# Kernel optimization log

Hardware: AMD Instinct MI355X
Metric: run time of the kernel (lower is better)

The kernel has to match this reference:

```python
import jax, jax.numpy as jnp
import numpy as np

B, S, E, H = 2, 2048, 1024, 16
D = E // H  # head_dim = 64


def setup_inputs() -> dict:
    key = jax.random.key(0)
    ks = jax.random.split(key, 12)
    sc = 1.0 / np.sqrt(E)
    inp = {
        "query": jax.random.normal(ks[0], (B, S, E), jnp.float32),
        "key": jax.random.normal(ks[1], (B, S, E), jnp.float32),
        "value": jax.random.normal(ks[2], (B, S, E), jnp.float32),
        # causal mask: 1 where attending is allowed, 0 where blocked
        "mask": jnp.tril(jnp.ones((S, S), jnp.int32))[None, None, :, :],
        "Wq": jax.random.normal(ks[3], (E, E), jnp.float32) * sc,
        "bq": jax.random.normal(ks[4], (E,), jnp.float32) * sc,
        "Wk": jax.random.normal(ks[5], (E, E), jnp.float32) * sc,
        "bk": jax.random.normal(ks[6], (E,), jnp.float32) * sc,
        "Wv": jax.random.normal(ks[7], (E, E), jnp.float32) * sc,
        "bv": jax.random.normal(ks[8], (E,), jnp.float32) * sc,
        "Wo": jax.random.normal(ks[9], (E, E), jnp.float32) * sc,
        "bo": jax.random.normal(ks[10], (E,), jnp.float32) * sc,
    }
    return inp


def reference(query, key, value, mask, Wq, bq, Wk, bk, Wv, bv, Wo, bo):
    scale = jnp.asarray(np.sqrt(D), query.dtype)
    # Linear projections (torch Linear: x @ W.T + b)
    Q = query @ Wq.T + bq
    K = key @ Wk.T + bk
    V = value @ Wv.T + bv
    # [B, S, E] -> [B, H, S, D]
    Q = Q.reshape(B, -1, H, D).transpose(0, 2, 1, 3)
    K = K.reshape(B, -1, H, D).transpose(0, 2, 1, 3)
    V = V.reshape(B, -1, H, D).transpose(0, 2, 1, 3)
    # full [B, H, Sq, Sk] score matrix, as in the source
    scores = jnp.einsum("bhqd,bhkd->bhqk", Q, K) / scale
    scores = jnp.where(mask == 0, jnp.asarray(-1e10, scores.dtype), scores)
    weights = jax.nn.softmax(scores, axis=-1)
    weighted = jnp.einsum("bhqk,bhkd->bhqd", weights, V)
    concat = weighted.transpose(0, 2, 1, 3).reshape(B, -1, E)
    return concat @ Wo.T + bo
```

## Files before the change

### kernel.cpp

```cpp
#include <hip/hip_runtime.h>
#include <math.h>

#define BB 2
#define SS 2048
#define EE 1024
#define HH 16
#define DD 64

typedef unsigned short u16;
typedef __attribute__((ext_vector_type(8))) short short8;
typedef __attribute__((ext_vector_type(4))) float f32x4;

__device__ __forceinline__ u16 f2bf(float x) {
    union { float f; unsigned u; } v; v.f = x;
    return (u16)((v.u + 0x7fffu + ((v.u >> 16) & 1u)) >> 16);
}

__device__ __forceinline__ float exp2_fast(float x) {
    float r;
    asm("v_exp_f32 %0, %1" : "=v"(r) : "v"(x));
    return r;
}

#define GLL16(gp, lp) \
    __builtin_amdgcn_global_load_lds( \
        (const __attribute__((address_space(1))) void*)(gp), \
        (__attribute__((address_space(3))) void*)(lp), 16, 0, 0)

#define BARRIER do { asm volatile("" ::: "memory"); \
                     __builtin_amdgcn_s_barrier();  \
                     asm volatile("" ::: "memory"); } while (0)
#define VMW4 asm volatile("s_waitcnt vmcnt(4)" ::: "memory")
#define VMW0 asm volatile("s_waitcnt vmcnt(0)" ::: "memory")
#define LG0  asm volatile("s_waitcnt lgkmcnt(0)" ::: "memory")
#define SCHED0 __builtin_amdgcn_sched_barrier(0)

#define QSCALE 0.18033688f

__global__ __launch_bounds__(256)
void cvt_bf16(const float* __restrict__ s0, const float* __restrict__ s1,
              const float* __restrict__ s2, const float* __restrict__ s3,
              u16* __restrict__ d0, u16* __restrict__ d1,
              u16* __restrict__ d2, u16* __restrict__ d3)
{
    const int z = blockIdx.y;
    const float* s; u16* d;
    switch (z) {
        case 0: s = s0; d = d0; break;
        case 1: s = s1; d = d1; break;
        case 2: s = s2; d = d2; break;
        default: s = s3; d = d3; break;
    }
    const int i = (blockIdx.x * 256 + threadIdx.x) * 8;
    float4 a = *(const float4*)(s + i);
    float4 b = *(const float4*)(s + i + 4);
    short8 r;
    r[0] = (short)f2bf(a.x); r[1] = (short)f2bf(a.y);
    r[2] = (short)f2bf(a.z); r[3] = (short)f2bf(a.w);
    r[4] = (short)f2bf(b.x); r[5] = (short)f2bf(b.y);
    r[6] = (short)f2bf(b.z); r[7] = (short)f2bf(b.w);
    *(short8*)(d + i) = r;
}

__global__ __launch_bounds__(256, 3)
void gemm_qkv(const float* __restrict__ Xq, const float* __restrict__ Xk,
              const float* __restrict__ Xv,
              const u16* __restrict__ Wqb, const u16* __restrict__ Wkb,
              const u16* __restrict__ Wvb,
              const float* __restrict__ bq, const float* __restrict__ bk,
              const float* __restrict__ bv,
              u16* __restrict__ Qh, u16* __restrict__ Kh, u16* __restrict__ Vth)
{
    __shared__ __align__(16) u16 LS[2][2][128][32];
#define LA (LS[0])
#define LB (LS[1])

    const int bid = blockIdx.x;
    const int swz = (bid & 7) * 96 + (bid >> 3);
    const int z   = swz >> 8;
    const int rem = swz & 255;
    const int m0  = (rem >> 3) * 128;
    const int n0  = (rem & 7) * 128;

    const float* X = (z == 0) ? Xq : (z == 1) ? Xk : Xv;
    const u16* Wt = (z == 0) ? Wqb : (z == 1) ? Wkb : Wvb;
    const float* bias = (z == 0) ? bq : (z == 1) ? bk : bv;
    u16* out = (z == 0) ? Qh : (z == 1) ? Kh : Vth;

    const int t = threadIdx.x;
    const int w = t >> 6, l = t & 63;
    const int ln = l & 15, hi = l >> 4;
    const int wr = w >> 1, wc = w & 1;

    const int ar = t >> 1, ah = t & 1;
    const float* Xrow = X + (size_t)(m0 + ar) * 1024 + ah * 16;
    const int fa   = (ar >> 1) & 3;
    const int gpa0 = (2 * ah)     ^ fa;
    const int gpa1 = (2 * ah + 1) ^ fa;

    const int brow = t >> 2, gp4 = t & 3;
    const int gl4  = gp4 ^ (brow & 3);
    const u16* Wp0 = Wt + (size_t)(n0 + brow) * 1024 + gl4 * 8;
    const u16* Wp1 = Wt + (size_t)(n0 + 64 + brow) * 1024 + gl4 * 8;

    f32x4 acc[4][4];
    #pragma unroll
    for (int i = 0; i < 4; i++)
        #pragma unroll
        for (int j = 0; j < 4; j++)
            acc[i][j] = (f32x4){0.f, 0.f, 0.f, 0.f};

    float4 e0, e1, e2, e3;
    float4 o0, o1, o2, o3;

#define ISSUE_B(buf, k0_) {                                                  \
        GLL16(Wp0 + (k0_), &LB[buf][brow][gp4 * 8]);                         \
        GLL16(Wp1 + (k0_), &LB[buf][brow + 64][gp4 * 8]);                    \
    }
#define LOAD_A(S0, S1, S2, S3, k0_) {                                        \
        S0 = *(const float4*)(Xrow + (k0_));                                 \
        S1 = *(const float4*)(Xrow + (k0_) + 4);                             \
        S2 = *(const float4*)(Xrow + (k0_) + 8);                             \
        S3 = *(const float4*)(Xrow + (k0_) + 12);                            \
    }
#define CVT_A(buf, S0, S1, S2, S3) {                                         \
        uint4 u0, u1;                                                        \
        u0.x = f2bf(S0.x) | ((unsigned)f2bf(S0.y) << 16);                    \
        u0.y = f2bf(S0.z) | ((unsigned)f2bf(S0.w) << 16);                    \
        u0.z = f2bf(S1.x) | ((unsigned)f2bf(S1.y) << 16);                    \
        u0.w = f2bf(S1.z) | ((unsigned)f2bf(S1.w) << 16);                    \
        u1.x = f2bf(S2.x) | ((unsigned)f2bf(S2.y) << 16);                    \
        u1.y = f2bf(S2.z) | ((unsigned)f2bf(S2.w) << 16);                    \
        u1.z = f2bf(S3.x) | ((unsigned)f2bf(S3.y) << 16);                    \
        u1.w = f2bf(S3.z) | ((unsigned)f2bf(S3.w) << 16);                    \
        *(uint4*)&LA[buf][ar][gpa0 * 8] = u0;                                \
        *(uint4*)&LA[buf][ar][gpa1 * 8] = u1;                                \
    }
#define COMPUTE(la_, lb_, SW) {                                              \
        _Pragma("unroll")                                                    \
        for (int mi = 0; mi < 4; mi++)                                       \
            af[mi] = *(const short8*)&LA[la_][wr*64 + mi*16 + ln]            \
                         [(hi ^ ((ln >> 1) & 3)) * 8];                       \
        _Pragma("unroll")                                                    \
        for (int nj = 0; nj < 4; nj++)                                       \
            bf[nj] = *(const short8*)&LB[lb_][wc*64 + nj*16 + ln]            \
                         [(hi ^ (ln & 3)) * 8];                              \
        _Pragma("unroll")                                                    \
        for (int mi = 0; mi < 4; mi++)                                       \
            _Pragma("unroll")                                                \
            for (int nj = 0; nj < 4; nj++)                                   \
                acc[mi][nj] = (SW)                                           \
                    ? __builtin_amdgcn_mfma_f32_16x16x32_bf16(               \
                          bf[nj], af[mi], acc[mi][nj], 0, 0, 0)              \
                    : __builtin_amdgcn_mfma_f32_16x16x32_bf16(               \
                          af[mi], bf[nj], acc[mi][nj], 0, 0, 0);             \
    }
#define PIPELINE(SW)                                                         \
    LOAD_A(e0, e1, e2, e3, 0);                                               \
    CVT_A(0, e0, e1, e2, e3);                                                \
    ISSUE_B(0, 0); SCHED0;                                                   \
    LOAD_A(o0, o1, o2, o3, 32); SCHED0;                                      \
    VMW4; LG0; BARRIER;                                                      \
    for (int it = 0; it < 15; ++it) {                                        \
        const int k0 = it * 64;                                              \
        ISSUE_B(1, k0 + 32); SCHED0;                                         \
        LOAD_A(e0, e1, e2, e3, k0 + 64); SCHED0;                             \
        COMPUTE(0, 0, SW);                                                   \
        CVT_A(1, o0, o1, o2, o3);                                            \
        VMW4; LG0; BARRIER;                                                  \
        ISSUE_B(0, k0 + 64); SCHED0;                                         \
        LOAD_A(o0, o1, o2, o3, k0 + 96); SCHED0;                             \
        COMPUTE(1, 1, SW);                                                   \
        CVT_A(0, e0, e1, e2, e3);                                            \
        VMW4; LG0; BARRIER;                                                  \
    }                                                                        \
    ISSUE_B(1, 992); SCHED0;                                                 \
    COMPUTE(0, 0, SW);                                                       \
    CVT_A(1, o0, o1, o2, o3);                                                \
    VMW0; LG0; BARRIER;                                                      \
    COMPUTE(1, 1, SW);

    short8 af[4], bf[4];

    if (z == 2) { PIPELINE(0) } else { PIPELINE(1) }
#undef ISSUE_B
#undef LOAD_A
#undef CVT_A
#undef COMPUTE
#undef PIPELINE

    u16* T = &LS[0][0][0][0];
    const int b = m0 >> 11;

    if (z == 2) {
        #pragma unroll
        for (int mi = 0; mi < 4; mi++) {
            #pragma unroll
            for (int nj = 0; nj < 4; nj++) {
                const int nc = wc * 64 + nj * 16 + ln;
                const float bv2 = bias[n0 + nc];
                const int sr0 = wr * 64 + mi * 16 + hi * 4;
                uint2 pk;
                pk.x = f2bf(acc[mi][nj][0] + bv2)
                     | ((unsigned)f2bf(acc[mi][nj][1] + bv2) << 16);
                pk.y = f2bf(acc[mi][nj][2] + bv2)
                     | ((unsigned)f2bf(acc[mi][nj][3] + bv2) << 16);
                const int gp = (sr0 >> 2) ^ (nc & 31);
                *(uint2*)&T[nc * 128 + gp * 4] = pk;
            }
        }
        __syncthreads();
        const int s0 = m0 & 2047;
        const int sidx = t & 15;
        const int ncr0 = t >> 4;
        #pragma unroll
        for (int i = 0; i < 8; i++) {
            const int nc = ncr0 + i * 16;
            const int a  = sidx * 2;
            const int pa = a ^ (nc & 31);
            const int pb = (a + 1) ^ (nc & 31);
            uint2 lo  = *(const uint2*)&T[nc * 128 + pa * 4];
            uint2 hi2 = *(const uint2*)&T[nc * 128 + pb * 4];
            uint4 vd = make_uint4(lo.x, lo.y, hi2.x, hi2.y);
            const int h = (n0 >> 6) + (nc >> 6);
            const int d = nc & 63;
            *(uint4*)&out[(((size_t)(b * HH + h) * 64 + d) << 11) + s0 + sidx * 8] = vd;
        }
    } else {
        #pragma unroll
        for (int mi = 0; mi < 4; mi++) {
            const int s = (m0 & 2047) + wr * 64 + mi * 16 + ln;
            #pragma unroll
            for (int nj = 0; nj < 4; nj++) {
                const int ncb = wc * 64 + nj * 16 + hi * 4;
                float4 b4 = *(const float4*)&bias[n0 + ncb];
                float v0 = acc[mi][nj][0] + b4.x;
                float v1 = acc[mi][nj][1] + b4.y;
                float v2 = acc[mi][nj][2] + b4.z;
                float v3 = acc[mi][nj][3] + b4.w;
                if (z == 0) {
                    v0 *= QSCALE; v1 *= QSCALE; v2 *= QSCALE; v3 *= QSCALE;
                }
                const int h  = (n0 + ncb) >> 6;
                const int d0 = ncb & 63;
                uint2 pk;
                pk.x = f2bf(v0) | ((unsigned)f2bf(v1) << 16);
                pk.y = f2bf(v2) | ((unsigned)f2bf(v3) << 16);
                *(uint2*)&out[((((size_t)(b * HH + h)) << 11) + s) * 64 + d0] = pk;
            }
        }
    }
#undef LA
#undef LB
}

__global__ __launch_bounds__(256)
void gemm_out(const u16* __restrict__ Xb, const u16* __restrict__ Wb,
              const float* __restrict__ bias, float* __restrict__ outp)
{
    __shared__ __align__(16) u16 As[2][64][32];
    __shared__ __align__(16) u16 Bs[2][128][32];

    const int bid = blockIdx.x;
    const int swz = (bid & 7) * 64 + (bid >> 3);
    const int m0  = (swz >> 3) * 64;
    const int n0  = (swz & 7) * 128;

    const int t = threadIdx.x;
    const int w = t >> 6, l = t & 63;
    const int ln = l & 15, hi = l >> 4;
    const int wr = w >> 1, wc = w & 1;

    const int row0 = t >> 2, gp4 = t & 3;
    const int gl4  = gp4 ^ (row0 & 3);

    f32x4 acc[2][4];
    #pragma unroll
    for (int i = 0; i < 2; i++)
        #pragma unroll
        for (int j = 0; j < 4; j++)
            acc[i][j] = (f32x4){0.f, 0.f, 0.f, 0.f};

#define OSTAGE(buf, k0_) { \
    GLL16(Xb + (size_t)(m0 + row0) * 1024 + (k0_) + gl4 * 8,        \
          &As[buf][row0][gp4 * 8]);                                  \
    GLL16(Wb + (size_t)(n0 + row0) * 1024 + (k0_) + gl4 * 8,        \
          &Bs[buf][row0][gp4 * 8]);                                  \
    GLL16(Wb + (size_t)(n0 + 64 + row0) * 1024 + (k0_) + gl4 * 8,   \
          &Bs[buf][row0 + 64][gp4 * 8]); }

    OSTAGE(0, 0);
    __syncthreads();
    int cur = 0;
    for (int k0 = 0; k0 < 1024; k0 += 32) {
        if (k0 + 32 < 1024) OSTAGE(cur ^ 1, k0 + 32);
        short8 af[2], bfr[4];
        #pragma unroll
        for (int mi = 0; mi < 2; mi++)
            af[mi] = *(const short8*)&As[cur][wr*32 + mi*16 + ln][(hi ^ (ln & 3))*8];
        #pragma unroll
        for (int nj = 0; nj < 4; nj++)
            bfr[nj] = *(const short8*)&Bs[cur][wc*64 + nj*16 + ln][(hi ^ (ln & 3))*8];
        #pragma unroll
        for (int mi = 0; mi < 2; mi++)
            #pragma unroll
            for (int nj = 0; nj < 4; nj++)
                acc[mi][nj] = __builtin_amdgcn_mfma_f32_16x16x32_bf16(
                    bfr[nj], af[mi], acc[mi][nj], 0, 0, 0);
        __syncthreads();
        cur ^= 1;
    }
#undef OSTAGE

    #pragma unroll
    for (int mi = 0; mi < 2; mi++) {
        const int m = m0 + wr * 32 + mi * 16 + ln;
        #pragma unroll
        for (int nj = 0; nj < 4; nj++) {
            const int nb0 = n0 + wc * 64 + nj * 16 + hi * 4;
            float4 b4 = *(const float4*)&bias[nb0];
            float4 st;
            st.x = acc[mi][nj][0] + b4.x;
            st.y = acc[mi][nj][1] + b4.y;
            st.z = acc[mi][nj][2] + b4.z;
            st.w = acc[mi][nj][3] + b4.w;
            *(float4*)&outp[(size_t)m * 1024 + nb0] = st;
        }
    }
}

__global__ __launch_bounds__(256)
void attn_mfma(const u16* __restrict__ Qh, const u16* __restrict__ Kh,
               const u16* __restrict__ Vt, u16* __restrict__ Cc)
{
    __shared__ __align__(16) u16 Ks[2][2][4][64][8];
    __shared__ __align__(16) u16 Vs[2][2][4][64][8];
    __shared__ __align__(16) u16 Ps[4][16][64];
    const int bh = blockIdx.x;
    const int y  = 31 - blockIdx.y;
    const int q0 = y * 64;
    const int t = threadIdx.x, w = t >> 6, l = t & 63;
    const int ln = l & 15, hi = l >> 4;
    const size_t base = (size_t)bh * SS * DD;
    const int qg = q0 + w * 16 + ln;

    short8 qf0, qf1;
    {
        const u16* qp = Qh + base + (size_t)qg * 64 + hi * 8;
        qf0 = *(const short8*)qp;
        qf1 = *(const short8*)(qp + 32);
    }
    f32x4 o[4];
    #pragma unroll
    for (int dj = 0; dj < 4; dj++) o[dj] = (f32x4){0.f, 0.f, 0.f, 0.f};
    float mrun = -INFINITY, lrun = 0.f;

#define STAGE(buf, key0_)                                                        \
    {                                                                            \
        _Pragma("unroll")                                                        \
        for (int i_ = 0; i_ < 4; i_++) {                                         \
            const int id_ = w + i_ * 4;                                          \
            if (id_ < 8) {                                                       \
                const int dc_ = id_ >> 2, kg_ = id_ & 3;                         \
                const u16* gp_ = Kh + base + (size_t)((key0_) + l) * 64          \
                                 + dc_ * 32 + kg_ * 8;                           \
                GLL16(gp_, &Ks[buf][dc_][kg_][0][0]);                            \
            } else {                                                             \
                const int kc_ = (id_ >> 2) & 1, kg_ = id_ & 3;                   \
                const u16* gp_ = Vt + base + (size_t)l * SS + (key0_)            \
                                 + kc_ * 32 + kg_ * 8;                           \
                GLL16(gp_, &Vs[buf][kc_][kg_][0][0]);                            \
            }                                                                    \
        }                                                                        \
    }

    STAGE(0, 0);
    __syncthreads();
    int cur = 0;
    const int nkt = y + 1;
    for (int kt = 0; kt < nkt; kt++) {
        const int key0 = kt * 64;
        if (kt + 1 < nkt) STAGE(cur ^ 1, key0 + 64);

        f32x4 st[4];
        __builtin_amdgcn_s_setprio(1);
        #pragma unroll
        for (int kt4 = 0; kt4 < 4; kt4++) {
            short8 ka = *(const short8*)&Ks[cur][0][hi][kt4 * 16 + ln][0];
            short8 kb = *(const short8*)&Ks[cur][1][hi][kt4 * 16 + ln][0];
            f32x4 zz = (f32x4){0.f, 0.f, 0.f, 0.f};
            zz = __builtin_amdgcn_mfma_f32_16x16x32_bf16(ka, qf0, zz, 0, 0, 0);
            zz = __builtin_amdgcn_mfma_f32_16x16x32_bf16(kb, qf1, zz, 0, 0, 0);
            st[kt4] = zz;
        }
        __builtin_amdgcn_s_setprio(0);
        if (kt == y) {
            #pragma unroll
            for (int kt4 = 0; kt4 < 4; kt4++)
                #pragma unroll
                for (int r = 0; r < 4; r++)
                    if (key0 + kt4 * 16 + hi * 4 + r > qg)
                        st[kt4][r] = -INFINITY;
        }

        float tmax = -INFINITY;
        #pragma unroll
        for (int kt4 = 0; kt4 < 4; kt4++)
            #pragma unroll
            for (int r = 0; r < 4; r++)
                tmax = fmaxf(tmax, st[kt4][r]);
        tmax = fmaxf(tmax, __shfl_xor(tmax, 16));
        tmax = fmaxf(tmax, __shfl_xor(tmax, 32));
        if (__ballot(tmax > mrun + 8.f)) {
            const float mnew = fmaxf(mrun, tmax);
            const float alpha = exp2_fast(mrun - mnew);
            lrun *= alpha;
            mrun = mnew;
            #pragma unroll
            for (int r = 0; r < 4; r++) {
                const float ar = __shfl(alpha, hi * 4 + r);
                #pragma unroll
                for (int dj = 0; dj < 4; dj++) o[dj][r] *= ar;
            }
        }
        float p[4][4];
        float lsum = 0.f;
        #pragma unroll
        for (int kt4 = 0; kt4 < 4; kt4++)
            #pragma unroll
            for (int r = 0; r < 4; r++) {
                p[kt4][r] = exp2_fast(st[kt4][r] - mrun);
                lsum += p[kt4][r];
            }
        lsum += __shfl_xor(lsum, 16);
        lsum += __shfl_xor(lsum, 32);
        lrun += lsum;

        char* prow = ((char*)Ps) + (w * 16 + ln) * 128 + (hi & 1) * 8;
        #pragma unroll
        for (int kt4 = 0; kt4 < 4; kt4++) {
            unsigned dw0, dw1;
            asm("v_cvt_pk_bf16_f32 %0, %1, %2" : "=v"(dw0)
                : "v"(p[kt4][0]), "v"(p[kt4][1]));
            asm("v_cvt_pk_bf16_f32 %0, %1, %2" : "=v"(dw1)
                : "v"(p[kt4][2]), "v"(p[kt4][3]));
            const int g = (2 * kt4 + (hi >> 1)) ^ (ln & 7);
            *(uint2*)(prow + g * 16) = make_uint2(dw0, dw1);
        }

        __builtin_amdgcn_s_setprio(1);
        #pragma unroll
        for (int kc = 0; kc < 2; kc++) {
            const int gr = (kc * 4 + hi) ^ (ln & 7);
            short8 pa = *(const short8*)(((char*)Ps) + (w * 16 + ln) * 128 + gr * 16);
            #pragma unroll
            for (int dj = 0; dj < 4; dj++) {
                short8 vb = *(const short8*)&Vs[cur][kc][hi][dj * 16 + ln][0];
                o[dj] = __builtin_amdgcn_mfma_f32_16x16x32_bf16(pa, vb, o[dj], 0, 0, 0);
            }
        }
        __builtin_amdgcn_s_setprio(0);
        __syncthreads();
        cur ^= 1;
    }
#undef STAGE

    const float inv = 1.f / lrun;
    #pragma unroll
    for (int r = 0; r < 4; r++) {
        const float ir = __shfl(inv, hi * 4 + r);
        const int s = q0 + w * 16 + hi * 4 + r;
        const size_t ob = ((size_t)(bh >> 4) * SS + s) * EE + (bh & 15) * 64;
        #pragma unroll
        for (int dj = 0; dj < 4; dj++)
            Cc[ob + dj * 16 + ln] = f2bf(o[dj][r] * ir);
    }
}

extern "C" void kernel_launch(void* const* d_in, const int* in_sizes, int n_in,
                              void* d_out, int out_size, void* d_ws, size_t ws_size,
                              hipStream_t stream)
{
    (void)in_sizes; (void)n_in; (void)out_size; (void)ws_size;
    const float* query = (const float*)d_in[0];
    const float* key   = (const float*)d_in[1];
    const float* value = (const float*)d_in[2];
    const float* Wq = (const float*)d_in[4];
    const float* bq = (const float*)d_in[5];
    const float* Wk = (const float*)d_in[6];
    const float* bk = (const float*)d_in[7];
    const float* Wv = (const float*)d_in[8];
    const float* bv = (const float*)d_in[9];
    const float* Wo = (const float*)d_in[10];
    const float* bo = (const float*)d_in[11];
    float* out = (float*)d_out;

    char* ws = (char*)d_ws;
    u16* Wqb = (u16*)(ws + 25165824);
    u16* Wkb = (u16*)(ws + 27262976);
    u16* Wvb = (u16*)(ws + 29360128);
    u16* Wob = (u16*)(ws + 31457280);
    u16* Qh  = (u16*)(ws + 33554432);
    u16* Kh  = (u16*)(ws + 41943040);
    u16* Vth = (u16*)(ws + 50331648);
    u16* Cc  = (u16*)(ws + 58720256);

    cvt_bf16<<<dim3(512, 4), 256, 0, stream>>>(
        Wq, Wk, Wv, Wo, Wqb, Wkb, Wvb, Wob);

    gemm_qkv<<<768, 256, 0, stream>>>(
        query, key, value, Wqb, Wkb, Wvb, bq, bk, bv, Qh, Kh, Vth);
    attn_mfma<<<dim3(32, 32), 256, 0, stream>>>(Qh, Kh, Vth, Cc);
    gemm_out<<<512, 256, 0, stream>>>(Cc, Wob, bo, out);
}
```

Before: 118.8 us.

## Process two 64-row query tiles per attention block to reuse K/V tiles

Each attention workgroup now handles 128 query rows: every wave keeps two 16-row Q fragments, two online-softmax states and two output accumulators. Each staged K/V tile is then reused for twice as many MFMAs, halving global/LDS staging per unit of work. Block-to-tile mapping is reordered to interleave long and short causal rows for load balance. The grid halves to 512 blocks and per-thread register use roughly doubles, which may lower occupancy and leave fewer blocks than CUs for latency hiding.

```diff
diff --git a/kernel.cpp b/kernel.cpp
--- a/kernel.cpp
+++ b/kernel.cpp
@@ -335,25 +335,34 @@
 {
     __shared__ __align__(16) u16 Ks[2][2][4][64][8];
     __shared__ __align__(16) u16 Vs[2][2][4][64][8];
-    __shared__ __align__(16) u16 Ps[4][16][64];
+    __shared__ __align__(16) u16 Ps[4][2][16][64];
     const int bh = blockIdx.x;
-    const int y  = 31 - blockIdx.y;
-    const int q0 = y * 64;
+    const int by = blockIdx.y;
+    const int y  = (by < 8) ? (15 - 2 * by) : (2 * (by - 8));
+    const int q0 = y * 128;
     const int t = threadIdx.x, w = t >> 6, l = t & 63;
     const int ln = l & 15, hi = l >> 4;
     const size_t base = (size_t)bh * SS * DD;
-    const int qg = q0 + w * 16 + ln;
-
-    short8 qf0, qf1;
+    const int qga = q0 + w * 16 + ln;
+    const int qgb = qga + 64;
+
+    short8 qf0, qf1, qf2, qf3;
     {
-        const u16* qp = Qh + base + (size_t)qg * 64 + hi * 8;
+        const u16* qp = Qh + base + (size_t)qga * 64 + hi * 8;
         qf0 = *(const short8*)qp;
         qf1 = *(const short8*)(qp + 32);
-    }
-    f32x4 o[4];
+        const u16* qp2 = qp + (size_t)64 * 64;
+        qf2 = *(const short8*)qp2;
+        qf3 = *(const short8*)(qp2 + 32);
+    }
+    f32x4 oa[4], ob[4];
     #pragma unroll
-    for (int dj = 0; dj < 4; dj++) o[dj] = (f32x4){0.f, 0.f, 0.f, 0.f};
-    float mrun = -INFINITY, lrun = 0.f;
+    for (int dj = 0; dj < 4; dj++) {
+        oa[dj] = (f32x4){0.f, 0.f, 0.f, 0.f};
+        ob[dj] = (f32x4){0.f, 0.f, 0.f, 0.f};
+    }
+    float m0r = -INFINITY, l0r = 0.f;
+    float m1r = -INFINITY, l1r = 0.f;
 
 #define STAGE(buf, key0_)                                                        \
     {                                                                            \
@@ -377,86 +386,109 @@
     STAGE(0, 0);
     __syncthreads();
     int cur = 0;
-    const int nkt = y + 1;
+    const int nkt = 2 * y + 2;
     for (int kt = 0; kt < nkt; kt++) {
         const int key0 = kt * 64;
         if (kt + 1 < nkt) STAGE(cur ^ 1, key0 + 64);
 
-        f32x4 st[4];
+        f32x4 st0[4], st1[4];
         __builtin_amdgcn_s_setprio(1);
         #pragma unroll
         for (int kt4 = 0; kt4 < 4; kt4++) {
             short8 ka = *(const short8*)&Ks[cur][0][hi][kt4 * 16 + ln][0];
             short8 kb = *(const short8*)&Ks[cur][1][hi][kt4 * 16 + ln][0];
-            f32x4 zz = (f32x4){0.f, 0.f, 0.f, 0.f};
-            zz = __builtin_amdgcn_mfma_f32_16x16x32_bf16(ka, qf0, zz, 0, 0, 0);
-            zz = __builtin_amdgcn_mfma_f32_16x16x32_bf16(kb, qf1, zz, 0, 0, 0);
-            st[kt4] = zz;
+            f32x4 z0 = (f32x4){0.f, 0.f, 0.f, 0.f};
+            z0 = __builtin_amdgcn_mfma_f32_16x16x32_bf16(ka, qf0, z0, 0, 0, 0);
+            z0 = __builtin_amdgcn_mfma_f32_16x16x32_bf16(kb, qf1, z0, 0, 0, 0);
+            st0[kt4] = z0;
+            f32x4 z1 = (f32x4){0.f, 0.f, 0.f, 0.f};
+            z1 = __builtin_amdgcn_mfma_f32_16x16x32_bf16(ka, qf2, z1, 0, 0, 0);
+            z1 = __builtin_amdgcn_mfma_f32_16x16x32_bf16(kb, qf3, z1, 0, 0, 0);
+            st1[kt4] = z1;
         }
         __builtin_amdgcn_s_setprio(0);
-        if (kt == y) {
+
+        if (kt >= nkt - 2) {
             #pragma unroll
             for (int kt4 = 0; kt4 < 4; kt4++)
                 #pragma unroll
-                for (int r = 0; r < 4; r++)
-                    if (key0 + kt4 * 16 + hi * 4 + r > qg)
-                        st[kt4][r] = -INFINITY;
-        }
-
-        float tmax = -INFINITY;
+                for (int r = 0; r < 4; r++) {
+                    const int key = key0 + kt4 * 16 + hi * 4 + r;
+                    if (key > qga) st0[kt4][r] = -INFINITY;
+                    if (key > qgb) st1[kt4][r] = -INFINITY;
+                }
+        }
+
+        float t0 = -INFINITY, t1 = -INFINITY;
         #pragma unroll
         for (int kt4 = 0; kt4 < 4; kt4++)
             #pragma unroll
-            for (int r = 0; r < 4; r++)
-                tmax = fmaxf(tmax, st[kt4][r]);
-        tmax = fmaxf(tmax, __shfl_xor(tmax, 16));
-        tmax = fmaxf(tmax, __shfl_xor(tmax, 32));
-        if (__ballot(tmax > mrun + 8.f)) {
-            const float mnew = fmaxf(mrun, tmax);
-            const float alpha = exp2_fast(mrun - mnew);
-            lrun *= alpha;
-            mrun = mnew;
-            #pragma unroll
             for (int r = 0; r < 4; r++) {
-                const float ar = __shfl(alpha, hi * 4 + r);
+                t0 = fmaxf(t0, st0[kt4][r]);
+                t1 = fmaxf(t1, st1[kt4][r]);
+            }
+        t0 = fmaxf(t0, __shfl_xor(t0, 16));
+        t0 = fmaxf(t0, __shfl_xor(t0, 32));
+        t1 = fmaxf(t1, __shfl_xor(t1, 16));
+        t1 = fmaxf(t1, __shfl_xor(t1, 32));
+        if (__ballot((t0 > m0r + 8.f) || (t1 > m1r + 8.f))) {
+            const float mn0 = fmaxf(m0r, t0);
+            const float mn1 = fmaxf(m1r, t1);
+            const float a0 = exp2_fast(m0r - mn0);
+            const float a1 = exp2_fast(m1r - mn1);
+            l0r *= a0; l1r *= a1;
+            m0r = mn0; m1r = mn1;
+            #pragma unroll
+            for (int r = 0; r < 4; r++) {
+                const float ar0 = __shfl(a0, hi * 4 + r);
+                const float ar1 = __shfl(a1, hi * 4 + r);
                 #pragma unroll
-                for (int dj = 0; dj < 4; dj++) o[dj][r] *= ar;
+                for (int dj = 0; dj < 4; dj++) {
+                    oa[dj][r] *= ar0;
+                    ob[dj][r] *= ar1;
+                }
             }
         }
-        float p[4][4];
-        float lsum = 0.f;
-        #pragma unroll
-        for (int kt4 = 0; kt4 < 4; kt4++)
+        float lsum0 = 0.f, lsum1 = 0.f;
+        char* prow0 = ((char*)&Ps[w][0][0][0]) + ln * 128 + (hi & 1) * 8;
+        char* prow1 = ((char*)&Ps[w][1][0][0]) + ln * 128 + (hi & 1) * 8;
+        #pragma unroll
+        for (int kt4 = 0; kt4 < 4; kt4++) {
+            float p0[4], p1[4];
             #pragma unroll
             for (int r = 0; r < 4; r++) {
-                p[kt4][r] = exp2_fast(st[kt4][r] - mrun);
-                lsum += p[kt4][r];
+                p0[r] = exp2_fast(st0[kt4][r] - m0r);
+                p1[r] = exp2_fast(st1[kt4][r] - m1r);
+                lsum0 += p0[r];
+                lsum1 += p1[r];
             }
-        lsum += __shfl_xor(lsum, 16);
-        lsum += __shfl_xor(lsum, 32);
-        lrun += lsum;
-
-        char* prow = ((char*)Ps) + (w * 16 + ln) * 128 + (hi & 1) * 8;
-        #pragma unroll
-        for (int kt4 = 0; kt4 < 4; kt4++) {
-            unsigned dw0, dw1;
-            asm("v_cvt_pk_bf16_f32 %0, %1, %2" : "=v"(dw0)
-                : "v"(p[kt4][0]), "v"(p[kt4][1]));
-            asm("v_cvt_pk_bf16_f32 %0, %1, %2" : "=v"(dw1)
-                : "v"(p[kt4][2]), "v"(p[kt4][3]));
+            unsigned dw0, dw1, dw2, dw3;
+            asm("v_cvt_pk_bf16_f32 %0, %1, %2" : "=v"(dw0) : "v"(p0[0]), "v"(p0[1]));
+            asm("v_cvt_pk_bf16_f32 %0, %1, %2" : "=v"(dw1) : "v"(p0[2]), "v"(p0[3]));
+            asm("v_cvt_pk_bf16_f32 %0, %1, %2" : "=v"(dw2) : "v"(p1[0]), "v"(p1[1]));
+            asm("v_cvt_pk_bf16_f32 %0, %1, %2" : "=v"(dw3) : "v"(p1[2]), "v"(p1[3]));
             const int g = (2 * kt4 + (hi >> 1)) ^ (ln & 7);
-            *(uint2*)(prow + g * 16) = make_uint2(dw0, dw1);
-        }
+            *(uint2*)(prow0 + g * 16) = make_uint2(dw0, dw1);
+            *(uint2*)(prow1 + g * 16) = make_uint2(dw2, dw3);
+        }
+        lsum0 += __shfl_xor(lsum0, 16);
+        lsum0 += __shfl_xor(lsum0, 32);
+        lsum1 += __shfl_xor(lsum1, 16);
+        lsum1 += __shfl_xor(lsum1, 32);
+        l0r += lsum0;
+        l1r += lsum1;
 
         __builtin_amdgcn_s_setprio(1);
         #pragma unroll
         for (int kc = 0; kc < 2; kc++) {
             const int gr = (kc * 4 + hi) ^ (ln & 7);
-            short8 pa = *(const short8*)(((char*)Ps) + (w * 16 + ln) * 128 + gr * 16);
+            short8 pa0 = *(const short8*)(((char*)&Ps[w][0][0][0]) + ln * 128 + gr * 16);
+            short8 pa1 = *(const short8*)(((char*)&Ps[w][1][0][0]) + ln * 128 + gr * 16);
             #pragma unroll
             for (int dj = 0; dj < 4; dj++) {
                 short8 vb = *(const short8*)&Vs[cur][kc][hi][dj * 16 + ln][0];
-                o[dj] = __builtin_amdgcn_mfma_f32_16x16x32_bf16(pa, vb, o[dj], 0, 0, 0);
+                oa[dj] = __builtin_amdgcn_mfma_f32_16x16x32_bf16(pa0, vb, oa[dj], 0, 0, 0);
+                ob[dj] = __builtin_amdgcn_mfma_f32_16x16x32_bf16(pa1, vb, ob[dj], 0, 0, 0);
             }
         }
         __builtin_amdgcn_s_setprio(0);
@@ -465,15 +497,20 @@
     }
 #undef STAGE
 
-    const float inv = 1.f / lrun;
+    const float inv0 = 1.f / l0r;
+    const float inv1 = 1.f / l1r;
     #pragma unroll
     for (int r = 0; r < 4; r++) {
-        const float ir = __shfl(inv, hi * 4 + r);
+        const float ir0 = __shfl(inv0, hi * 4 + r);
+        const float ir1 = __shfl(inv1, hi * 4 + r);
         const int s = q0 + w * 16 + hi * 4 + r;
-        const size_t ob = ((size_t)(bh >> 4) * SS + s) * EE + (bh & 15) * 64;
-        #pragma unroll
-        for (int dj = 0; dj < 4; dj++)
-            Cc[ob + dj * 16 + ln] = f2bf(o[dj][r] * ir);
+        const size_t ob0 = ((size_t)(bh >> 4) * SS + s) * EE + (bh & 15) * 64;
+        const size_t ob1 = ((size_t)(bh >> 4) * SS + s + 64) * EE + (bh & 15) * 64;
+        #pragma unroll
+        for (int dj = 0; dj < 4; dj++) {
+            Cc[ob0 + dj * 16 + ln] = f2bf(oa[dj][r] * ir0);
+            Cc[ob1 + dj * 16 + ln] = f2bf(ob[dj][r] * ir1);
+        }
     }
 }
 
@@ -510,6 +547,6 @@
 
     gemm_qkv<<<768, 256, 0, stream>>>(
         query, key, value, Wqb, Wkb, Wvb, bq, bk, bv, Qh, Kh, Vth);
-    attn_mfma<<<dim3(32, 32), 256, 0, stream>>>(Qh, Kh, Vth, Cc);
+    attn_mfma<<<dim3(32, 16), 256, 0, stream>>>(Qh, Kh, Vth, Cc);
     gemm_out<<<512, 256, 0, stream>>>(Cc, Wob, bo, out);
 }
```

After: 123.0 us. +3.5%, slower.

## Deepen QKV GEMM pipeline to triple-buffered B tiles and three A register stages

Applied to the files above, without the earlier changes.

Restructures the QKV projection GEMM main loop from a double-buffered scheme to triple-buffered LDS for the weight tile, with three sets of fp32 A-operand registers. Global loads are issued further ahead, and vmcnt waits are relaxed so more memory traffic stays in flight behind the MFMA work. In exchange it uses more registers and LDS per block, which may reduce occupancy under the 3-blocks-per-CU launch bound. The loop is fully restaged with a 6-step rotation and a hand-written epilogue.

```diff
diff --git a/kernel.cpp b/kernel.cpp
--- a/kernel.cpp
+++ b/kernel.cpp
@@ -30,9 +30,10 @@
 #define BARRIER do { asm volatile("" ::: "memory"); \
                      __builtin_amdgcn_s_barrier();  \
                      asm volatile("" ::: "memory"); } while (0)
-#define VMW4 asm volatile("s_waitcnt vmcnt(4)" ::: "memory")
-#define VMW0 asm volatile("s_waitcnt vmcnt(0)" ::: "memory")
-#define LG0  asm volatile("s_waitcnt lgkmcnt(0)" ::: "memory")
+#define VMW10 asm volatile("s_waitcnt vmcnt(10)" ::: "memory")
+#define VMW6  asm volatile("s_waitcnt vmcnt(6)" ::: "memory")
+#define VMW0  asm volatile("s_waitcnt vmcnt(0)" ::: "memory")
+#define LG0   asm volatile("s_waitcnt lgkmcnt(0)" ::: "memory")
 #define SCHED0 __builtin_amdgcn_sched_barrier(0)
 
 #define QSCALE 0.18033688f
@@ -71,9 +72,10 @@
               const float* __restrict__ bv,
               u16* __restrict__ Qh, u16* __restrict__ Kh, u16* __restrict__ Vth)
 {
-    __shared__ __align__(16) u16 LS[2][2][128][32];
-#define LA (LS[0])
-#define LB (LS[1])
+    __shared__ __align__(16) u16 LS[20480];
+    typedef u16 tile_t[128][32];
+    tile_t* LA = (tile_t*)&LS[0];
+    tile_t* LB = (tile_t*)&LS[8192];
 
     const int bid = blockIdx.x;
     const int swz = (bid & 7) * 96 + (bid >> 3);
@@ -112,6 +114,7 @@
 
     float4 e0, e1, e2, e3;
     float4 o0, o1, o2, o3;
+    float4 p0, p1, p2, p3;
 
 #define ISSUE_B(buf, k0_) {                                                  \
         GLL16(Wp0 + (k0_), &LB[buf][brow][gp4 * 8]);                         \
@@ -155,29 +158,45 @@
                     : __builtin_amdgcn_mfma_f32_16x16x32_bf16(               \
                           af[mi], bf[nj], acc[mi][nj], 0, 0, 0);             \
     }
+#define BODY(LAc, LBc, LBn, CLA, C0,C1,C2,C3, L0,L1,L2,L3, kB, kL, SW)       \
+    ISSUE_B(LBn, kB); SCHED0;                                                \
+    COMPUTE(LAc, LBc, SW);                                                   \
+    CVT_A(CLA, C0, C1, C2, C3);                                              \
+    LOAD_A(L0, L1, L2, L3, kL); SCHED0;                                      \
+    VMW10; LG0; BARRIER;
+
 #define PIPELINE(SW)                                                         \
     LOAD_A(e0, e1, e2, e3, 0);                                               \
     CVT_A(0, e0, e1, e2, e3);                                                \
-    ISSUE_B(0, 0); SCHED0;                                                   \
-    LOAD_A(o0, o1, o2, o3, 32); SCHED0;                                      \
-    VMW4; LG0; BARRIER;                                                      \
-    for (int it = 0; it < 15; ++it) {                                        \
-        const int k0 = it * 64;                                              \
-        ISSUE_B(1, k0 + 32); SCHED0;                                         \
-        LOAD_A(e0, e1, e2, e3, k0 + 64); SCHED0;                             \
-        COMPUTE(0, 0, SW);                                                   \
-        CVT_A(1, o0, o1, o2, o3);                                            \
-        VMW4; LG0; BARRIER;                                                  \
-        ISSUE_B(0, k0 + 64); SCHED0;                                         \
-        LOAD_A(o0, o1, o2, o3, k0 + 96); SCHED0;                             \
-        COMPUTE(1, 1, SW);                                                   \
-        CVT_A(0, e0, e1, e2, e3);                                            \
-        VMW4; LG0; BARRIER;                                                  \
+    ISSUE_B(0, 0);                                                           \
+    ISSUE_B(1, 32); SCHED0;                                                  \
+    LOAD_A(o0, o1, o2, o3, 32);                                              \
+    LOAD_A(p0, p1, p2, p3, 64); SCHED0;                                      \
+    VMW10; LG0; BARRIER;                                                     \
+    for (int it = 0; it < 4; ++it) {                                         \
+        const int kb = it * 192;                                             \
+        BODY(0,0, 2, 1, o0,o1,o2,o3, e0,e1,e2,e3, kb+64,  kb+96,  SW)        \
+        BODY(1,1, 0, 0, p0,p1,p2,p3, o0,o1,o2,o3, kb+96,  kb+128, SW)        \
+        BODY(0,2, 1, 1, e0,e1,e2,e3, p0,p1,p2,p3, kb+128, kb+160, SW)        \
+        BODY(1,0, 2, 0, o0,o1,o2,o3, e0,e1,e2,e3, kb+160, kb+192, SW)        \
+        BODY(0,1, 0, 1, p0,p1,p2,p3, o0,o1,o2,o3, kb+192, kb+224, SW)        \
+        BODY(1,2, 1, 0, e0,e1,e2,e3, p0,p1,p2,p3, kb+224, kb+256, SW)        \
     }                                                                        \
+    BODY(0,0, 2, 1, o0,o1,o2,o3, e0,e1,e2,e3, 832, 864, SW)         \
+    BODY(1,1, 0, 0, p0,p1,p2,p3, o0,o1,o2,o3, 864, 896, SW)         \
+    BODY(0,2, 1, 1, e0,e1,e2,e3, p0,p1,p2,p3, 896, 928, SW)         \
+    BODY(1,0, 2, 0, o0,o1,o2,o3, e0,e1,e2,e3, 928, 960, SW)         \
+    BODY(0,1, 0, 1, p0,p1,p2,p3, o0,o1,o2,o3, 960, 992, SW)         \
+                        \
     ISSUE_B(1, 992); SCHED0;                                                 \
+    COMPUTE(1, 2, SW);                                                       \
+    CVT_A(0, e0, e1, e2, e3);                                                \
+    VMW6; LG0; BARRIER;                                                      \
+                                          \
     COMPUTE(0, 0, SW);                                                       \
     CVT_A(1, o0, o1, o2, o3);                                                \
     VMW0; LG0; BARRIER;                                                      \
+                                                                    \
     COMPUTE(1, 1, SW);
 
     short8 af[4], bf[4];
@@ -187,9 +206,10 @@
 #undef LOAD_A
 #undef CVT_A
 #undef COMPUTE
+#undef BODY
 #undef PIPELINE
 
-    u16* T = &LS[0][0][0][0];
+    u16* T = &LS[0];
     const int b = m0 >> 11;
 
     if (z == 2) {
@@ -250,8 +270,6 @@
             }
         }
     }
-#undef LA
-#undef LB
 }
 
 __global__ __launch_bounds__(256)
```

Measured after the change: 133.9 us. 12.8% more time.
